# Performance work log

Hardware: AMD Instinct MI355X
Metric: run time of the kernel (lower is better)

Reference implementation:

```python
import jax, jax.numpy as jnp
import numpy as np

N = 100000
E = 1600000
IN_DIM, HID, Z = 128, 64, 32


def gcn_conv(x, src, dst, num_nodes, W, b):
    """PyG GCNConv: add self-loops, symmetric deg^-1/2 normalization.
    x: [N, F_in]; src/dst: [E] int (self-loops already appended by caller wrapper).
    """
    h = x @ W  # [N, F_out] transform first (PyG order)
    ones = jnp.ones(src.shape[0], dtype=x.dtype)
    deg = jax.ops.segment_sum(ones, dst, num_segments=num_nodes)  # in-degree incl. self-loop
    dinv = jnp.where(deg > 0, jax.lax.rsqrt(deg), 0.0)
    norm = dinv[src] * dinv[dst]  # [E]
    msgs = h[src] * norm[:, None]  # [E, F_out] irregular gather
    out = jax.ops.segment_sum(msgs, dst, num_segments=num_nodes)  # scatter-add
    return out + b


def setup_inputs() -> dict:
    key = jax.random.key(0)
    ks = jax.random.split(key, 10)
    x = jax.random.normal(ks[0], (N, IN_DIM), dtype=jnp.float32)
    edge_index = jax.random.randint(ks[1], (2, E), 0, N, dtype=jnp.int64)

    def glorot(k, fan_in, fan_out):
        s = jnp.sqrt(6.0 / (fan_in + fan_out))
        return jax.random.uniform(k, (fan_in, fan_out), jnp.float32, -s, s)

    return {
        "x": x,
        "edge_index": edge_index,
        "W1": glorot(ks[2], IN_DIM, HID),
        "b1": jnp.zeros((HID,), jnp.float32),
        "W2": glorot(ks[3], HID, Z),
        "b2": jnp.zeros((Z,), jnp.float32),
        "Wmu": glorot(ks[4], Z, Z),
        "bmu": jnp.zeros((Z,), jnp.float32),
        "Wlv": glorot(ks[5], Z, Z),
        "blv": jnp.zeros((Z,), jnp.float32),
    }


def reference(x, edge_index, W1, b1, W2, b2, Wmu, bmu, Wlv, blv):
    num_nodes = x.shape[0]
    loop = jnp.arange(num_nodes, dtype=edge_index.dtype)
    src = jnp.concatenate([edge_index[0], loop])  # self-loops appended
    dst = jnp.concatenate([edge_index[1], loop])
    h = jax.nn.relu(gcn_conv(x, src, dst, num_nodes, W1, b1))
    h = gcn_conv(h, src, dst, num_nodes, W2, b2)
    mu = h @ Wmu + bmu
    logvar = h @ Wlv + blv
    return (mu, logvar)
```

## Files before the change

### kernel.cpp

```cpp
#include <hip/hip_runtime.h>

#define N_NODES 100000
#define N_EDGES 1600000
#define IN_F   128
#define HID_F  64
#define Z_F    32
#define NBUK   782
#define BCAP   3072
#define P1T    4096
#define P1_BLOCKS ((N_EDGES + P1T - 1) / P1T)
#define AGG_CAP 2048

typedef unsigned int uint32;
typedef __attribute__((ext_vector_type(8))) short bf16x8;
typedef __attribute__((ext_vector_type(4))) float f32x4;

__device__ __forceinline__ unsigned short f2bf(float f) {
    unsigned u = __float_as_uint(f);
    u = (u + 0x7FFF + ((u >> 16) & 1)) >> 16;
    return (unsigned short)u;
}
__device__ __forceinline__ uint32 pack2bf(float lo, float hi) {
    return (uint32)f2bf(lo) | ((uint32)f2bf(hi) << 16);
}
__device__ __forceinline__ float bflo(uint32 u) { return __uint_as_float(u << 16); }
__device__ __forceinline__ float bfhi(uint32 u) { return __uint_as_float(u & 0xFFFF0000u); }

#define ACC8(u) { a0 += bflo(u.x); a1 += bfhi(u.x); a2 += bflo(u.y); a3 += bfhi(u.y); \
                  a4 += bflo(u.z); a5 += bfhi(u.z); a6 += bflo(u.w); a7 += bfhi(u.w); }

__global__ __launch_bounds__(256) void phase1_kernel(const int* __restrict__ ei,
                                                     int* __restrict__ gcur,
                                                     uint32* __restrict__ pairs,
                                                     const float* __restrict__ W1,
                                                     const float* __restrict__ W2,
                                                     const float* __restrict__ Wmu,
                                                     const float* __restrict__ Wlv,
                                                     unsigned short* __restrict__ Wt1,
                                                     unsigned short* __restrict__ Wt2,
                                                     unsigned short* __restrict__ Wth) {
    if (blockIdx.x == P1_BLOCKS) {
        int t = threadIdx.x;
        for (int i = t; i < IN_F * HID_F; i += 256) {
            int n = i >> 7, k = i & 127;
            Wt1[i] = f2bf(W1[k * HID_F + n]);
        }
        for (int i = t; i < HID_F * Z_F; i += 256) {
            int n = i >> 6, k = i & 63;
            Wt2[i] = f2bf(W2[k * Z_F + n]);
        }
        for (int i = t; i < Z_F * 64; i += 256) {
            int n = i >> 5, k = i & 31;
            Wth[i] = f2bf(n < 32 ? Wmu[k * Z_F + n] : Wlv[k * Z_F + (n - 32)]);
        }
        return;
    }
    __shared__ int hist[NBUK];
    __shared__ int lbase[NBUK];
    __shared__ int gbase[NBUK];
    __shared__ int lcur[NBUK];
    __shared__ uint32 stage[P1T];
    __shared__ unsigned short sbid[P1T];
    __shared__ int part[256];
    int tid = threadIdx.x;
    int e0 = blockIdx.x * P1T;
    int ecnt = N_EDGES - e0; if (ecnt > P1T) ecnt = P1T;
    for (int b = tid; b < NBUK; b += 256) { hist[b] = 0; lcur[b] = 0; }
    __syncthreads();
    int myd[16];
#pragma unroll
    for (int i = 0; i < 16; i++) {
        int k = tid + i * 256;
        myd[i] = (k < ecnt) ? ei[N_EDGES + e0 + k] : -1;
    }
#pragma unroll
    for (int i = 0; i < 16; i++)
        if (myd[i] >= 0) atomicAdd(&hist[myd[i] >> 7], 1);
    __syncthreads();
    int t4 = tid * 4;
    int l0 = 0, l1 = 0, l2 = 0, l3 = 0, s = 0;
    if (t4 + 0 < NBUK) { l0 = hist[t4 + 0]; s += l0; }
    if (t4 + 1 < NBUK) { l1 = hist[t4 + 1]; s += l1; }
    if (t4 + 2 < NBUK) { l2 = hist[t4 + 2]; s += l2; }
    if (t4 + 3 < NBUK) { l3 = hist[t4 + 3]; s += l3; }
    part[tid] = s;
    __syncthreads();
    for (int off = 1; off < 256; off <<= 1) {
        int add = (tid >= off) ? part[tid - off] : 0;
        __syncthreads();
        part[tid] += add;
        __syncthreads();
    }
    int run = part[tid] - s;
    if (t4 + 0 < NBUK) { lbase[t4 + 0] = run; run += l0; }
    if (t4 + 1 < NBUK) { lbase[t4 + 1] = run; run += l1; }
    if (t4 + 2 < NBUK) { lbase[t4 + 2] = run; run += l2; }
    if (t4 + 3 < NBUK) { lbase[t4 + 3] = run; run += l3; }
    for (int b = tid; b < NBUK; b += 256) {
        int h = hist[b];
        gbase[b] = h ? atomicAdd(&gcur[b], h) : 0;
    }
    __syncthreads();
#pragma unroll
    for (int i = 0; i < 16; i++) {
        int k = tid + i * 256;
        if (k < ecnt) {
            int sN = ei[e0 + k];
            int d  = myd[i];
            int b = d >> 7;
            int slot = lbase[b] + atomicAdd(&lcur[b], 1);
            stage[slot] = (uint32)sN | ((uint32)(d & 127) << 17);
            sbid[slot] = (unsigned short)b;
        }
    }
    __syncthreads();
    for (int k = tid; k < ecnt; k += 256) {
        int b = sbid[k];
        int r = gbase[b] + (k - lbase[b]);
        if (r < BCAP) pairs[(size_t)b * BCAP + r] = stage[k];
    }
}

__global__ __launch_bounds__(256) void phase2_kernel(const uint32* __restrict__ pairs,
                                                     const int* __restrict__ gcur,
                                                     int* __restrict__ rowptr,
                                                     float* __restrict__ dinv,
                                                     int* __restrict__ col) {
    __shared__ int lhist[128];
    __shared__ int lscan[128];
    __shared__ int lcur[128];
    __shared__ int stage[BCAP];
    __shared__ int wsum[4];
    int b = blockIdx.x;
    int tid = threadIdx.x;
    int cnt_b = gcur[b];
    if (cnt_b > BCAP) cnt_b = BCAP;
    int partial = 0;
    for (int i = tid; i < b; i += 256) partial += gcur[i];
#pragma unroll
    for (int off = 32; off > 0; off >>= 1) partial += __shfl_down(partial, off);
    if (tid < 128) { lhist[tid] = 0; lcur[tid] = 0; }
    if ((tid & 63) == 0) wsum[tid >> 6] = partial;
    __syncthreads();
    int gbase = wsum[0] + wsum[1] + wsum[2] + wsum[3];
    int node0 = b << 7;
    int nb = N_NODES - node0;
    if (nb > 128) nb = 128;
    const uint32* pb = pairs + (size_t)b * BCAP;
    for (int k = tid; k < cnt_b; k += 256) atomicAdd(&lhist[pb[k] >> 17], 1);
    __syncthreads();
    int v = (tid < 128) ? lhist[tid] : 0;
    if (tid < 128) lscan[tid] = v;
    __syncthreads();
    for (int off = 1; off < 128; off <<= 1) {
        int add = (tid < 128 && tid >= off) ? lscan[tid - off] : 0;
        __syncthreads();
        if (tid < 128) lscan[tid] += add;
        __syncthreads();
    }
    if (tid < 128) lscan[tid] -= v;
    __syncthreads();
    if (tid < nb) {
        rowptr[node0 + tid] = gbase + lscan[tid];
        dinv[node0 + tid] = rsqrtf((float)(lhist[tid] + 1));
    }
    if (b == NBUK - 1 && tid == 0) rowptr[N_NODES] = N_EDGES;
    for (int k = tid; k < cnt_b; k += 256) {
        uint32 u = pb[k];
        int ld = u >> 17;
        int r = atomicAdd(&lcur[ld], 1);
        stage[lscan[ld] + r] = (int)(u & 0x1FFFF);
    }
    __syncthreads();
    for (int k = tid; k < cnt_b; k += 256) col[gbase + k] = stage[k];
}

__global__ __launch_bounds__(256) void gemm1_kernel(const float* __restrict__ x,
                                                    const unsigned short* __restrict__ Wt1,
                                                    const float* __restrict__ dinv,
                                                    unsigned short* __restrict__ t1) {
    __shared__ unsigned short Cs[64 * 72];
    __shared__ float dv[64];
    int tid = threadIdx.x;
    int node0 = blockIdx.x * 64;
    if (tid < 64) {
        int n = node0 + tid;
        dv[tid] = (n < N_NODES) ? dinv[n] : 0.f;
    }
    __syncthreads();
    int w = tid >> 6, lane = tid & 63;
    int m = lane & 15, quad = lane >> 4;
    int row = w * 16 + m;
    int node = node0 + row;
    const float* xr = x + (size_t)min(node, N_NODES - 1) * IN_F;
    f32x4 acc0 = {0.f, 0.f, 0.f, 0.f};
    f32x4 acc1 = acc0, acc2 = acc0, acc3 = acc0;
#pragma unroll
    for (int ks = 0; ks < 4; ks++) {
        int kb = ks * 32 + quad * 8;
        float4 f0 = *(const float4*)(xr + kb);
        float4 f1 = *(const float4*)(xr + kb + 4);
        union { bf16x8 v; unsigned short u[8]; } A;
        A.u[0] = f2bf(f0.x); A.u[1] = f2bf(f0.y); A.u[2] = f2bf(f0.z); A.u[3] = f2bf(f0.w);
        A.u[4] = f2bf(f1.x); A.u[5] = f2bf(f1.y); A.u[6] = f2bf(f1.z); A.u[7] = f2bf(f1.w);
        bf16x8 b0 = *(const bf16x8*)&Wt1[(0 * 16 + m) * IN_F + kb];
        bf16x8 b1 = *(const bf16x8*)&Wt1[(1 * 16 + m) * IN_F + kb];
        bf16x8 b2 = *(const bf16x8*)&Wt1[(2 * 16 + m) * IN_F + kb];
        bf16x8 b3 = *(const bf16x8*)&Wt1[(3 * 16 + m) * IN_F + kb];
        acc0 = __builtin_amdgcn_mfma_f32_16x16x32_bf16(A.v, b0, acc0, 0, 0, 0);
        acc1 = __builtin_amdgcn_mfma_f32_16x16x32_bf16(A.v, b1, acc1, 0, 0, 0);
        acc2 = __builtin_amdgcn_mfma_f32_16x16x32_bf16(A.v, b2, acc2, 0, 0, 0);
        acc3 = __builtin_amdgcn_mfma_f32_16x16x32_bf16(A.v, b3, acc3, 0, 0, 0);
    }
    int rbase = w * 16 + quad * 4;
#pragma unroll
    for (int reg = 0; reg < 4; reg++) {
        int r = rbase + reg;
        float d = dv[r];
        Cs[r * 72 +  0 + m] = f2bf(acc0[reg] * d);
        Cs[r * 72 + 16 + m] = f2bf(acc1[reg] * d);
        Cs[r * 72 + 32 + m] = f2bf(acc2[reg] * d);
        Cs[r * 72 + 48 + m] = f2bf(acc3[reg] * d);
    }
    __syncthreads();
#pragma unroll
    for (int it = 0; it < 4; it++) {
        int idx = it * 256 + tid;
        int r = idx >> 4, c = idx & 15;
        int nd = node0 + r;
        if (nd < N_NODES) {
            uint2 vv = *(const uint2*)&Cs[r * 72 + c * 4];
            *(uint2*)&t1[(size_t)nd * HID_F + c * 4] = vv;
        }
    }
}

__global__ __launch_bounds__(256) void agg1gemm2_kernel(const unsigned short* __restrict__ t1,
                                                        const int* __restrict__ rowptr,
                                                        const int* __restrict__ col,
                                                        const float* __restrict__ dinv,
                                                        const float* __restrict__ b1,
                                                        const unsigned short* __restrict__ Wt2,
                                                        unsigned short* __restrict__ t2s) {
    __shared__ int lcol[AGG_CAP];
    __shared__ int lrp[65];
    __shared__ float ldv[64];
    __shared__ unsigned short h1s[64 * 72];
    __shared__ unsigned short Cs[64 * 36];
    int tid = threadIdx.x;
    int node0 = blockIdx.x * 64;
    if (tid < 65) lrp[tid] = rowptr[min(node0 + tid, N_NODES)];
    __syncthreads();
    int s0 = lrp[0];
    int cnt = lrp[64] - s0; if (cnt > AGG_CAP) cnt = AGG_CAP;
    for (int k = tid; k < cnt; k += 256) lcol[k] = col[s0 + k];
    if (tid < 64) {
        int n = node0 + tid;
        ldv[tid] = (n < N_NODES) ? dinv[n] : 0.f;
    }
    __syncthreads();
    int lane = tid & 63, w = tid >> 6;
    int grp = lane >> 3, fl = lane & 7;
    int gg = w * 8 + grp;
    const uint4* t1q = (const uint4*)t1;
    float4 bb0 = ((const float4*)b1)[fl * 2];
    float4 bb1 = ((const float4*)b1)[fl * 2 + 1];
#pragma unroll
    for (int rep = 0; rep < 2; rep++) {
        int li = gg + rep * 32;
        int node = node0 + li;
        uint4 pk = make_uint4(0u, 0u, 0u, 0u);
        if (node < N_NODES) {
            int s = lrp[li] - s0;
            int e = lrp[li + 1] - s0; if (e > cnt) e = cnt;
            float a0 = 0.f, a1 = 0.f, a2 = 0.f, a3 = 0.f;
            float a4 = 0.f, a5 = 0.f, a6 = 0.f, a7 = 0.f;
            int p = s;
            for (; p + 3 < e; p += 4) {
                int c0 = lcol[p], c1 = lcol[p + 1], c2 = lcol[p + 2], c3 = lcol[p + 3];
                uint4 u0 = t1q[(size_t)c0 * 8 + fl];
                uint4 u1 = t1q[(size_t)c1 * 8 + fl];
                uint4 u2 = t1q[(size_t)c2 * 8 + fl];
                uint4 u3 = t1q[(size_t)c3 * 8 + fl];
                ACC8(u0); ACC8(u1); ACC8(u2); ACC8(u3);
            }
            for (; p < e; p++) {
                uint4 u = t1q[(size_t)lcol[p] * 8 + fl];
                ACC8(u);
            }
            uint4 us = t1q[(size_t)node * 8 + fl];
            float di = ldv[li];
            float o0 = fmaxf(di * (a0 + bflo(us.x)) + bb0.x, 0.f);
            float o1 = fmaxf(di * (a1 + bfhi(us.x)) + bb0.y, 0.f);
            float o2 = fmaxf(di * (a2 + bflo(us.y)) + bb0.z, 0.f);
            float o3 = fmaxf(di * (a3 + bfhi(us.y)) + bb0.w, 0.f);
            float o4 = fmaxf(di * (a4 + bflo(us.z)) + bb1.x, 0.f);
            float o5 = fmaxf(di * (a5 + bfhi(us.z)) + bb1.y, 0.f);
            float o6 = fmaxf(di * (a6 + bflo(us.w)) + bb1.z, 0.f);
            float o7 = fmaxf(di * (a7 + bfhi(us.w)) + bb1.w, 0.f);
            pk.x = pack2bf(o0, o1);
            pk.y = pack2bf(o2, o3);
            pk.z = pack2bf(o4, o5);
            pk.w = pack2bf(o6, o7);
        }
        *(uint4*)&h1s[li * 72 + fl * 8] = pk;
    }
    __syncthreads();
    int m = lane & 15, quad = lane >> 4;
    int row = w * 16 + m;
    f32x4 acc0 = {0.f, 0.f, 0.f, 0.f};
    f32x4 acc1 = acc0;
#pragma unroll
    for (int ks = 0; ks < 2; ks++) {
        int kb = ks * 32 + quad * 8;
        bf16x8 a  = *(const bf16x8*)&h1s[row * 72 + kb];
        bf16x8 b0 = *(const bf16x8*)&Wt2[(0 * 16 + m) * HID_F + kb];
        bf16x8 b1v = *(const bf16x8*)&Wt2[(1 * 16 + m) * HID_F + kb];
        acc0 = __builtin_amdgcn_mfma_f32_16x16x32_bf16(a, b0, acc0, 0, 0, 0);
        acc1 = __builtin_amdgcn_mfma_f32_16x16x32_bf16(a, b1v, acc1, 0, 0, 0);
    }
    int rbase = w * 16 + quad * 4;
#pragma unroll
    for (int reg = 0; reg < 4; reg++) {
        int r = rbase + reg;
        float d = ldv[r];
        Cs[r * 36 +  0 + m] = f2bf(acc0[reg] * d);
        Cs[r * 36 + 16 + m] = f2bf(acc1[reg] * d);
    }
    __syncthreads();
#pragma unroll
    for (int it = 0; it < 2; it++) {
        int idx = it * 256 + tid;
        int r = idx >> 3, c = idx & 7;
        int nd = node0 + r;
        if (nd < N_NODES) {
            uint2 vv = *(const uint2*)&Cs[r * 36 + c * 4];
            *(uint2*)&t2s[(size_t)nd * Z_F + c * 4] = vv;
        }
    }
}

__global__ __launch_bounds__(256) void agg2heads_kernel(const unsigned short* __restrict__ t2s,
                                                        const int* __restrict__ rowptr,
                                                        const int* __restrict__ col,
                                                        const float* __restrict__ dinv,
                                                        const float* __restrict__ b2,
                                                        const unsigned short* __restrict__ Wth,
                                                        const float* __restrict__ bmu,
                                                        const float* __restrict__ blv,
                                                        float* __restrict__ out) {
    __shared__ int lcol[AGG_CAP];
    __shared__ int lrp[65];
    __shared__ float ldv[64];
    __shared__ unsigned short h2s[64 * 40];
    __shared__ float Cf[64 * 68];
    __shared__ float bias[64];
    int tid = threadIdx.x;
    int node0 = blockIdx.x * 64;
    if (tid < 65) lrp[tid] = rowptr[min(node0 + tid, N_NODES)];
    else if (tid >= 96 && tid < 128) bias[tid - 96] = bmu[tid - 96];
    else if (tid >= 128 && tid < 160) bias[tid - 96] = blv[tid - 128];
    __syncthreads();
    int s0 = lrp[0];
    int cnt = lrp[64] - s0; if (cnt > AGG_CAP) cnt = AGG_CAP;
    for (int k = tid; k < cnt; k += 256) lcol[k] = col[s0 + k];
    if (tid < 64) {
        int n = node0 + tid;
        ldv[tid] = (n < N_NODES) ? dinv[n] : 0.f;
    }
    __syncthreads();
    int lane = tid & 63, w = tid >> 6;
    int grp = lane >> 2, fo = lane & 3;
    int li = w * 16 + grp;
    const uint4* t2q = (const uint4*)t2s;
    float4 bb0 = ((const float4*)b2)[fo * 2];
    float4 bb1 = ((const float4*)b2)[fo * 2 + 1];
    {
        int node = node0 + li;
        uint4 pk = make_uint4(0u, 0u, 0u, 0u);
        if (node < N_NODES) {
            int s = lrp[li] - s0;
            int e = lrp[li + 1] - s0; if (e > cnt) e = cnt;
            float a0 = 0.f, a1 = 0.f, a2 = 0.f, a3 = 0.f;
            float a4 = 0.f, a5 = 0.f, a6 = 0.f, a7 = 0.f;
            int p = s;
            for (; p + 3 < e; p += 4) {
                int c0 = lcol[p], c1 = lcol[p + 1], c2 = lcol[p + 2], c3 = lcol[p + 3];
                uint4 u0 = t2q[(size_t)c0 * 4 + fo];
                uint4 u1 = t2q[(size_t)c1 * 4 + fo];
                uint4 u2 = t2q[(size_t)c2 * 4 + fo];
                uint4 u3 = t2q[(size_t)c3 * 4 + fo];
                ACC8(u0); ACC8(u1); ACC8(u2); ACC8(u3);
            }
            for (; p < e; p++) {
                uint4 u = t2q[(size_t)lcol[p] * 4 + fo];
                ACC8(u);
            }
            uint4 us = t2q[(size_t)node * 4 + fo];
            float di = ldv[li];
            float o0 = di * (a0 + bflo(us.x)) + bb0.x;
            float o1 = di * (a1 + bfhi(us.x)) + bb0.y;
            float o2 = di * (a2 + bflo(us.y)) + bb0.z;
            float o3 = di * (a3 + bfhi(us.y)) + bb0.w;
            float o4 = di * (a4 + bflo(us.z)) + bb1.x;
            float o5 = di * (a5 + bfhi(us.z)) + bb1.y;
            float o6 = di * (a6 + bflo(us.w)) + bb1.z;
            float o7 = di * (a7 + bfhi(us.w)) + bb1.w;
            pk.x = pack2bf(o0, o1);
            pk.y = pack2bf(o2, o3);
            pk.z = pack2bf(o4, o5);
            pk.w = pack2bf(o6, o7);
        }
        *(uint4*)&h2s[li * 40 + fo * 8] = pk;
    }
    __syncthreads();
    int m = lane & 15, quad = lane >> 4;
    int row = w * 16 + m;
    int kb = quad * 8;
    bf16x8 a  = *(const bf16x8*)&h2s[row * 40 + kb];
    bf16x8 b0 = *(const bf16x8*)&Wth[(0 * 16 + m) * Z_F + kb];
    bf16x8 b1 = *(const bf16x8*)&Wth[(1 * 16 + m) * Z_F + kb];
    bf16x8 b2v = *(const bf16x8*)&Wth[(2 * 16 + m) * Z_F + kb];
    bf16x8 b3 = *(const bf16x8*)&Wth[(3 * 16 + m) * Z_F + kb];
    f32x4 acc0 = {0.f, 0.f, 0.f, 0.f};
    f32x4 acc1 = acc0, acc2 = acc0, acc3 = acc0;
    acc0 = __builtin_amdgcn_mfma_f32_16x16x32_bf16(a, b0, acc0, 0, 0, 0);
    acc1 = __builtin_amdgcn_mfma_f32_16x16x32_bf16(a, b1, acc1, 0, 0, 0);
    acc2 = __builtin_amdgcn_mfma_f32_16x16x32_bf16(a, b2v, acc2, 0, 0, 0);
    acc3 = __builtin_amdgcn_mfma_f32_16x16x32_bf16(a, b3, acc3, 0, 0, 0);
    int rbase = w * 16 + quad * 4;
#pragma unroll
    for (int reg = 0; reg < 4; reg++) {
        int r = rbase + reg;
        Cf[r * 68 +  0 + m] = acc0[reg] + bias[ 0 + m];
        Cf[r * 68 + 16 + m] = acc1[reg] + bias[16 + m];
        Cf[r * 68 + 32 + m] = acc2[reg] + bias[32 + m];
        Cf[r * 68 + 48 + m] = acc3[reg] + bias[48 + m];
    }
    __syncthreads();
#pragma unroll
    for (int it = 0; it < 2; it++) {
        int idx = it * 256 + tid;
        int r = idx >> 3, c = idx & 7;
        int nd = node0 + r;
        if (nd < N_NODES) {
            float4 vmu = *(const float4*)&Cf[r * 68 + c * 4];
            float4 vlv = *(const float4*)&Cf[r * 68 + 32 + c * 4];
            *(float4*)&out[(size_t)nd * Z_F + c * 4] = vmu;
            *(float4*)&out[(size_t)N_NODES * Z_F + (size_t)nd * Z_F + c * 4] = vlv;
        }
    }
}

extern "C" void kernel_launch(void* const* d_in, const int* in_sizes, int n_in,
                              void* d_out, int out_size, void* d_ws, size_t ws_size,
                              hipStream_t stream) {
    const float* x   = (const float*)d_in[0];
    const int*   ei  = (const int*)d_in[1];
    const float* W1  = (const float*)d_in[2];
    const float* b1  = (const float*)d_in[3];
    const float* W2  = (const float*)d_in[4];
    const float* b2  = (const float*)d_in[5];
    const float* Wmu = (const float*)d_in[6];
    const float* bmu = (const float*)d_in[7];
    const float* Wlv = (const float*)d_in[8];
    const float* blv = (const float*)d_in[9];
    float* out = (float*)d_out;

    char* ws = (char*)d_ws;
    size_t off = 0;
    auto A = [&](size_t bytes) {
        size_t r = off;
        off += (bytes + 255) & ~(size_t)255;
        return r;
    };
    int*   gcur       = (int*)(ws + A((size_t)NBUK * 4));
    int*   rowptr     = (int*)(ws + A((size_t)(N_NODES + 1) * 4));
    float* dinv       = (float*)(ws + A((size_t)N_NODES * 4));
    unsigned short* Wt1 = (unsigned short*)(ws + A((size_t)IN_F * HID_F * 2));
    unsigned short* Wt2 = (unsigned short*)(ws + A((size_t)HID_F * Z_F * 2));
    unsigned short* Wth = (unsigned short*)(ws + A((size_t)Z_F * 64 * 2));
    int*   col        = (int*)(ws + A((size_t)N_EDGES * 4));
    char*  reg1 = ws + A((size_t)NBUK * BCAP * 4);
    uint32* pairs = (uint32*)reg1;
    unsigned short* t2s = (unsigned short*)reg1;
    unsigned short* t1 = (unsigned short*)(ws + A((size_t)N_NODES * HID_F * 2));

    hipMemsetAsync(gcur, 0, (size_t)NBUK * 4, stream);

    phase1_kernel<<<P1_BLOCKS + 1, 256, 0, stream>>>(ei, gcur, pairs,
                                                     W1, W2, Wmu, Wlv, Wt1, Wt2, Wth);
    phase2_kernel<<<NBUK, 256, 0, stream>>>(pairs, gcur, rowptr, dinv, col);

    int nblk = (N_NODES + 63) / 64;
    gemm1_kernel<<<nblk, 256, 0, stream>>>(x, Wt1, dinv, t1);
    agg1gemm2_kernel<<<nblk, 256, 0, stream>>>(t1, rowptr, col, dinv, b1, Wt2, t2s);
    agg2heads_kernel<<<nblk, 256, 0, stream>>>(t2s, rowptr, col, dinv, b2, Wth, bmu, blv, out);
}
```

Baseline: 213.5 us.

## Fuse CSR build phase with first GEMM via global degree counts

Phase1 now also accumulates per-node in-degree into a global deg array with atomics, which lets gemm1 compute dinv directly instead of waiting for phase2. Phase2 and gemm1 are merged into one launch with disjoint block ranges, so the CSR build and the first dense transform run concurrently and one launch is removed. Phase1 also processes twice as many edges per block. The cost is 1.6M extra global atomics, a larger memset, and higher register pressure in phase1.

```diff
diff --git a/kernel.cpp b/kernel.cpp
--- a/kernel.cpp
+++ b/kernel.cpp
@@ -7,9 +7,11 @@
 #define Z_F    32
 #define NBUK   782
 #define BCAP   3072
-#define P1T    4096
+#define P1T    8192
 #define P1_BLOCKS ((N_EDGES + P1T - 1) / P1T)
 #define AGG_CAP 2048
+#define DEG_PAD 100352
+#define G1_BLOCKS ((N_NODES + 63) / 64)
 
 typedef unsigned int uint32;
 typedef __attribute__((ext_vector_type(8))) short bf16x8;
@@ -32,6 +34,7 @@
 __global__ __launch_bounds__(256) void phase1_kernel(const int* __restrict__ ei,
                                                      int* __restrict__ gcur,
                                                      uint32* __restrict__ pairs,
+                                                     int* __restrict__ deg,
                                                      const float* __restrict__ W1,
                                                      const float* __restrict__ W2,
                                                      const float* __restrict__ Wmu,
@@ -67,15 +70,18 @@
     int ecnt = N_EDGES - e0; if (ecnt > P1T) ecnt = P1T;
     for (int b = tid; b < NBUK; b += 256) { hist[b] = 0; lcur[b] = 0; }
     __syncthreads();
-    int myd[16];
-#pragma unroll
-    for (int i = 0; i < 16; i++) {
+    int myd[32];
+#pragma unroll
+    for (int i = 0; i < 32; i++) {
         int k = tid + i * 256;
         myd[i] = (k < ecnt) ? ei[N_EDGES + e0 + k] : -1;
     }
 #pragma unroll
-    for (int i = 0; i < 16; i++)
-        if (myd[i] >= 0) atomicAdd(&hist[myd[i] >> 7], 1);
+    for (int i = 0; i < 32; i++)
+        if (myd[i] >= 0) {
+            atomicAdd(&hist[myd[i] >> 7], 1);
+            atomicAdd(&deg[myd[i]], 1);
+        }
     __syncthreads();
     int t4 = tid * 4;
     int l0 = 0, l1 = 0, l2 = 0, l3 = 0, s = 0;
@@ -102,7 +108,7 @@
     }
     __syncthreads();
 #pragma unroll
-    for (int i = 0; i < 16; i++) {
+    for (int i = 0; i < 32; i++) {
         int k = tid + i * 256;
         if (k < ecnt) {
             int sN = ei[e0 + k];
@@ -121,71 +127,71 @@
     }
 }
 
-__global__ __launch_bounds__(256) void phase2_kernel(const uint32* __restrict__ pairs,
-                                                     const int* __restrict__ gcur,
-                                                     int* __restrict__ rowptr,
-                                                     float* __restrict__ dinv,
-                                                     int* __restrict__ col) {
-    __shared__ int lhist[128];
-    __shared__ int lscan[128];
-    __shared__ int lcur[128];
-    __shared__ int stage[BCAP];
-    __shared__ int wsum[4];
-    int b = blockIdx.x;
+__global__ __launch_bounds__(256) void p2g1_kernel(const uint32* __restrict__ pairs,
+                                                   const int* __restrict__ gcur,
+                                                   int* __restrict__ rowptr,
+                                                   float* __restrict__ dinv,
+                                                   int* __restrict__ col,
+                                                   const float* __restrict__ x,
+                                                   const unsigned short* __restrict__ Wt1,
+                                                   const int* __restrict__ deg,
+                                                   unsigned short* __restrict__ t1) {
     int tid = threadIdx.x;
-    int cnt_b = gcur[b];
-    if (cnt_b > BCAP) cnt_b = BCAP;
-    int partial = 0;
-    for (int i = tid; i < b; i += 256) partial += gcur[i];
-#pragma unroll
-    for (int off = 32; off > 0; off >>= 1) partial += __shfl_down(partial, off);
-    if (tid < 128) { lhist[tid] = 0; lcur[tid] = 0; }
-    if ((tid & 63) == 0) wsum[tid >> 6] = partial;
-    __syncthreads();
-    int gbase = wsum[0] + wsum[1] + wsum[2] + wsum[3];
-    int node0 = b << 7;
-    int nb = N_NODES - node0;
-    if (nb > 128) nb = 128;
-    const uint32* pb = pairs + (size_t)b * BCAP;
-    for (int k = tid; k < cnt_b; k += 256) atomicAdd(&lhist[pb[k] >> 17], 1);
-    __syncthreads();
-    int v = (tid < 128) ? lhist[tid] : 0;
-    if (tid < 128) lscan[tid] = v;
-    __syncthreads();
-    for (int off = 1; off < 128; off <<= 1) {
-        int add = (tid < 128 && tid >= off) ? lscan[tid - off] : 0;
-        __syncthreads();
-        if (tid < 128) lscan[tid] += add;
-        __syncthreads();
-    }
-    if (tid < 128) lscan[tid] -= v;
-    __syncthreads();
-    if (tid < nb) {
-        rowptr[node0 + tid] = gbase + lscan[tid];
-        dinv[node0 + tid] = rsqrtf((float)(lhist[tid] + 1));
-    }
-    if (b == NBUK - 1 && tid == 0) rowptr[N_NODES] = N_EDGES;
-    for (int k = tid; k < cnt_b; k += 256) {
-        uint32 u = pb[k];
-        int ld = u >> 17;
-        int r = atomicAdd(&lcur[ld], 1);
-        stage[lscan[ld] + r] = (int)(u & 0x1FFFF);
-    }
-    __syncthreads();
-    for (int k = tid; k < cnt_b; k += 256) col[gbase + k] = stage[k];
-}
-
-__global__ __launch_bounds__(256) void gemm1_kernel(const float* __restrict__ x,
-                                                    const unsigned short* __restrict__ Wt1,
-                                                    const float* __restrict__ dinv,
-                                                    unsigned short* __restrict__ t1) {
+    if (blockIdx.x < NBUK) {
+        __shared__ int lhist[128];
+        __shared__ int lscan[128];
+        __shared__ int lcur[128];
+        __shared__ int stage[BCAP];
+        __shared__ int wsum[4];
+        int b = blockIdx.x;
+        int cnt_b = gcur[b];
+        if (cnt_b > BCAP) cnt_b = BCAP;
+        int partial = 0;
+        for (int i = tid; i < b; i += 256) partial += gcur[i];
+#pragma unroll
+        for (int off = 32; off > 0; off >>= 1) partial += __shfl_down(partial, off);
+        if (tid < 128) { lhist[tid] = 0; lcur[tid] = 0; }
+        if ((tid & 63) == 0) wsum[tid >> 6] = partial;
+        __syncthreads();
+        int gbase = wsum[0] + wsum[1] + wsum[2] + wsum[3];
+        int node0 = b << 7;
+        int nb = N_NODES - node0;
+        if (nb > 128) nb = 128;
+        const uint32* pb = pairs + (size_t)b * BCAP;
+        for (int k = tid; k < cnt_b; k += 256) atomicAdd(&lhist[pb[k] >> 17], 1);
+        __syncthreads();
+        int v = (tid < 128) ? lhist[tid] : 0;
+        if (tid < 128) lscan[tid] = v;
+        __syncthreads();
+        for (int off = 1; off < 128; off <<= 1) {
+            int add = (tid < 128 && tid >= off) ? lscan[tid - off] : 0;
+            __syncthreads();
+            if (tid < 128) lscan[tid] += add;
+            __syncthreads();
+        }
+        if (tid < 128) lscan[tid] -= v;
+        __syncthreads();
+        if (tid < nb) {
+            rowptr[node0 + tid] = gbase + lscan[tid];
+            dinv[node0 + tid] = rsqrtf((float)(lhist[tid] + 1));
+        }
+        if (b == NBUK - 1 && tid == 0) rowptr[N_NODES] = N_EDGES;
+        for (int k = tid; k < cnt_b; k += 256) {
+            uint32 u = pb[k];
+            int ld = u >> 17;
+            int r = atomicAdd(&lcur[ld], 1);
+            stage[lscan[ld] + r] = (int)(u & 0x1FFFF);
+        }
+        __syncthreads();
+        for (int k = tid; k < cnt_b; k += 256) col[gbase + k] = stage[k];
+        return;
+    }
     __shared__ unsigned short Cs[64 * 72];
     __shared__ float dv[64];
-    int tid = threadIdx.x;
-    int node0 = blockIdx.x * 64;
+    int node0 = (blockIdx.x - NBUK) * 64;
     if (tid < 64) {
         int n = node0 + tid;
-        dv[tid] = (n < N_NODES) ? dinv[n] : 0.f;
+        dv[tid] = (n < N_NODES) ? rsqrtf((float)(deg[n] + 1)) : 0.f;
     }
     __syncthreads();
     int w = tid >> 6, lane = tid & 63;
@@ -474,9 +480,10 @@
         off += (bytes + 255) & ~(size_t)255;
         return r;
     };
-    int*   gcur       = (int*)(ws + A((size_t)NBUK * 4));
-    int*   rowptr     = (int*)(ws + A((size_t)(N_NODES + 1) * 4));
-    float* dinv       = (float*)(ws + A((size_t)N_NODES * 4));
+    int*   deg   = (int*)(ws + A((size_t)DEG_PAD * 4));
+    int*   gcur  = (int*)(ws + A((size_t)NBUK * 4));
+    int*   rowptr = (int*)(ws + A((size_t)(N_NODES + 1) * 4));
+    float* dinv   = (float*)(ws + A((size_t)N_NODES * 4));
     unsigned short* Wt1 = (unsigned short*)(ws + A((size_t)IN_F * HID_F * 2));
     unsigned short* Wt2 = (unsigned short*)(ws + A((size_t)HID_F * Z_F * 2));
     unsigned short* Wth = (unsigned short*)(ws + A((size_t)Z_F * 64 * 2));
@@ -486,14 +493,12 @@
     unsigned short* t2s = (unsigned short*)reg1;
     unsigned short* t1 = (unsigned short*)(ws + A((size_t)N_NODES * HID_F * 2));
 
-    hipMemsetAsync(gcur, 0, (size_t)NBUK * 4, stream);
-
-    phase1_kernel<<<P1_BLOCKS + 1, 256, 0, stream>>>(ei, gcur, pairs,
+    hipMemsetAsync(deg, 0, (size_t)DEG_PAD * 4 + (size_t)NBUK * 4, stream);
+
+    phase1_kernel<<<P1_BLOCKS + 1, 256, 0, stream>>>(ei, gcur, pairs, deg,
                                                      W1, W2, Wmu, Wlv, Wt1, Wt2, Wth);
-    phase2_kernel<<<NBUK, 256, 0, stream>>>(pairs, gcur, rowptr, dinv, col);
-
-    int nblk = (N_NODES + 63) / 64;
-    gemm1_kernel<<<nblk, 256, 0, stream>>>(x, Wt1, dinv, t1);
-    agg1gemm2_kernel<<<nblk, 256, 0, stream>>>(t1, rowptr, col, dinv, b1, Wt2, t2s);
-    agg2heads_kernel<<<nblk, 256, 0, stream>>>(t2s, rowptr, col, dinv, b2, Wth, bmu, blv, out);
-}
+    p2g1_kernel<<<NBUK + G1_BLOCKS, 256, 0, stream>>>(pairs, gcur, rowptr, dinv, col,
+                                                      x, Wt1, deg, t1);
+    agg1gemm2_kernel<<<G1_BLOCKS, 256, 0, stream>>>(t1, rowptr, col, dinv, b1, Wt2, t2s);
+    agg2heads_kernel<<<G1_BLOCKS, 256, 0, stream>>>(t2s, rowptr, col, dinv, b2, Wth, bmu, blv, out);
+}
```

Result: slower. 269.7 us (+26.3%).
